# Optimization experiments

Hardware: AMD Instinct MI355X
Metric: run time of the kernel (lower is better)

Reference implementation:

```python
import jax, jax.numpy as jnp
import numpy as np

T, S, B, D, H, DH, DI = 1024, 1024, 4, 1024, 16, 64, 4096
SCALE = 1.0 / (DH ** 0.5)


def _ln(x, g, b, eps=1e-5):
    m = jnp.mean(x, axis=-1, keepdims=True)
    v = jnp.mean((x - m) ** 2, axis=-1, keepdims=True)
    return (x - m) * jax.lax.rsqrt(v + eps) * g + b


def setup_inputs() -> dict:
    key = jax.random.key(0)
    ks = jax.random.split(key, 16)
    s = 0.02
    inp = {
        "dec_inp": jax.random.normal(ks[0], (T, B, D), jnp.float32),
        "enc_out": jax.random.normal(ks[1], (T, B, D), jnp.float32),
        # causal mask for self-attn: [qlen, klen, bsz], True = masked
        "dec_mask": jnp.broadcast_to(jnp.triu(jnp.ones((T, T), bool), 1)[:, :, None], (T, T, B)),
        # encoder padding mask: [klen, bsz], last 128 positions padded
        "enc_mask": jnp.broadcast_to((jnp.arange(S) >= S - 128)[:, None], (S, B)),
        # self-attn params
        "W_q1": jax.random.normal(ks[2], (D, H * DH), jnp.float32) * s,
        "W_kv1": jax.random.normal(ks[3], (D, 2 * H * DH), jnp.float32) * s,
        "W_o1": jax.random.normal(ks[4], (H * DH, D), jnp.float32) * s,
        "g1": jnp.ones((D,), jnp.float32), "b1": jnp.zeros((D,), jnp.float32),
        # cross-attn params
        "W_q2": jax.random.normal(ks[5], (D, H * DH), jnp.float32) * s,
        "W_kv2": jax.random.normal(ks[6], (D, 2 * H * DH), jnp.float32) * s,
        "W_o2": jax.random.normal(ks[7], (H * DH, D), jnp.float32) * s,
        "g2": jnp.ones((D,), jnp.float32), "b2": jnp.zeros((D,), jnp.float32),
        # FFN params
        "W_ff1": jax.random.normal(ks[8], (D, DI), jnp.float32) * s,
        "b_ff1": jnp.zeros((DI,), jnp.float32),
        "W_ff2": jax.random.normal(ks[9], (DI, D), jnp.float32) * s,
        "b_ff2": jnp.zeros((D,), jnp.float32),
        "g3": jnp.ones((D,), jnp.float32), "b3": jnp.zeros((D,), jnp.float32),
    }
    return inp


def reference(dec_inp, enc_out, dec_mask, enc_mask,
              W_q1, W_kv1, W_o1, g1, b1,
              W_q2, W_kv2, W_o2, g2, b2,
              W_ff1, b_ff1, W_ff2, b_ff2, g3, b3):
    # ---- self-attention (MultiHeadAttn, pre_lnorm=True, mems=None) ----
    # NOTE: q is computed from the UN-normalized h; k,v from LN(c) — faithful to source.
    c = _ln(dec_inp, g1, b1)
    q = (dec_inp @ W_q1).reshape(T, B, H, DH)
    kv = (c @ W_kv1)
    k, v = jnp.split(kv, 2, axis=-1)
    k = k.reshape(T, B, H, DH)
    v = v.reshape(T, B, H, DH)
    score = jnp.einsum('ibnd,jbnd->ijbn', q, k) * SCALE  # [T,T,B,H]
    score = jnp.where(dec_mask[:, :, :, None], -jnp.inf, score)
    prob = jax.nn.softmax(score, axis=1)
    vec = jnp.einsum('ijbn,jbnd->ibnd', prob, v).reshape(T, B, H * DH)
    out1 = dec_inp + vec @ W_o1

    # ---- cross-attention (ContextMultiHeadAttn, pre_lnorm=True) ----
    # NOTE: residual uses the layer-normed h (source reassigns h = layer_norm(h)).
    h2 = _ln(out1, g2, b2)
    q2 = (h2 @ W_q2).reshape(T, B, H, DH)
    kv2 = enc_out @ W_kv2  # enc_out is NOT layer-normed in source
    k2, v2 = jnp.split(kv2, 2, axis=-1)
    k2 = k2.reshape(S, B, H, DH)
    v2 = v2.reshape(S, B, H, DH)
    score2 = jnp.einsum('ibnd,jbnd->ijbn', q2, k2) * SCALE  # [T,S,B,H]
    score2 = jnp.where(enc_mask[None, :, :, None], -10000.0, score2)
    prob2 = jax.nn.softmax(score2, axis=1)
    vec2 = jnp.einsum('ijbn,jbnd->ibnd', prob2, v2).reshape(T, B, H * DH)
    out2 = h2 + vec2 @ W_o2

    # ---- position-wise FFN (pre_lnorm) ----
    h3 = _ln(out2, g3, b3)
    core = jax.nn.gelu(h3 @ W_ff1 + b_ff1, approximate=False) @ W_ff2 + b_ff2
    return out2 + core
```

## Files before the change

### kernel.cpp

```cpp
#include <hip/hip_runtime.h>
#include <hip/hip_bf16.h>

#define T_ 1024
#define S_ 1024
#define B_ 4
#define D_ 1024
#define H_ 16
#define DH_ 64
#define DI_ 4096
#define NTOK 4096

typedef __attribute__((ext_vector_type(8))) short bf16x8;
typedef __attribute__((ext_vector_type(4))) float f32x4;

__device__ __forceinline__ short f2bf(float f) {
  unsigned u = __builtin_bit_cast(unsigned, f);
  u += 0x7fffu + ((u >> 16) & 1u);
  return (short)(u >> 16);
}

__device__ __forceinline__ void g2l16(const void* g, void* l) {
  __builtin_amdgcn_global_load_lds(
      (const __attribute__((address_space(1))) unsigned int*)g,
      (__attribute__((address_space(3))) unsigned int*)l, 16, 0, 0);
}

template <int EPI>
__global__ __launch_bounds__(256, 2) void gemm_bt(
    const short* __restrict__ A, const short* __restrict__ Bt,
    float* __restrict__ outF, short* __restrict__ outB,
    const float* __restrict__ res, const float* __restrict__ bias,
    short* __restrict__ Kgp, short* __restrict__ Vgp,
    int M, int N, int K) {
  __shared__ short sA[2][128 * 64];
  __shared__ short sB[2][128 * 64];
  const int tid = threadIdx.x;
  const int lane = tid & 63;
  const int w = tid >> 6;
  const int wr = w >> 1, wc = w & 1;
  const int r15 = lane & 15, g4 = lane >> 4;
  const size_t row0 = (size_t)blockIdx.x * 128;
  const size_t col0 = (size_t)blockIdx.y * 128;

  f32x4 acc[4][4];
#pragma unroll
  for (int i = 0; i < 4; i++)
#pragma unroll
    for (int j = 0; j < 4; j++) acc[i][j] = (f32x4){0.f, 0.f, 0.f, 0.f};

  auto stage = [&](int buf, int k0) {
#pragma unroll
    for (int i = 0; i < 4; i++) {
      int flat = i * 256 + tid;
      int row = flat >> 3;
      int gs = flat & 7;
      int col = k0 + ((gs ^ (row & 7)) << 3);
      g2l16(A + (row0 + row) * (size_t)K + col, &sA[buf][(i * 256 + w * 64) * 8]);
      g2l16(Bt + (col0 + row) * (size_t)K + col, &sB[buf][(i * 256 + w * 64) * 8]);
    }
  };

  stage(0, 0);
  __syncthreads();

  const int nk = K >> 6;
  for (int kt = 0; kt < nk; ++kt) {
    const int cur = kt & 1;
    if (kt + 1 < nk) stage(cur ^ 1, (kt + 1) << 6);
#pragma unroll
    for (int kk = 0; kk < 2; ++kk) {
      bf16x8 af[4], bfr[4];
#pragma unroll
      for (int mi = 0; mi < 4; mi++) {
        int rowA = wr * 64 + mi * 16 + r15;
        af[mi] = *(const bf16x8*)(&sA[cur][rowA * 64 +
                                           (((kk * 4 + g4) ^ (rowA & 7)) << 3)]);
        int rowB = wc * 64 + mi * 16 + r15;
        bfr[mi] = *(const bf16x8*)(&sB[cur][rowB * 64 +
                                            (((kk * 4 + g4) ^ (rowB & 7)) << 3)]);
      }
#pragma unroll
      for (int mi = 0; mi < 4; mi++)
#pragma unroll
        for (int ni = 0; ni < 4; ni++)
          acc[mi][ni] = __builtin_amdgcn_mfma_f32_16x16x32_bf16(af[mi], bfr[ni],
                                                                acc[mi][ni], 0, 0, 0);
    }
    __syncthreads();
  }

#pragma unroll
  for (int mi = 0; mi < 4; mi++) {
    size_t row = row0 + wr * 64 + mi * 16 + (g4 << 2);
#pragma unroll
    for (int ni = 0; ni < 4; ni++) {
      size_t col = col0 + wc * 64 + ni * 16 + r15;
      float bcol = (EPI == 2 || EPI == 3) ? bias[col] : 0.f;
#pragma unroll
      for (int r = 0; r < 4; r++) {
        size_t idx = (row + r) * (size_t)N + col;
        float v = acc[mi][ni][r];
        if (EPI == 0) {
          outB[idx] = f2bf(v);
        } else if (EPI == 1) {
          outF[idx] = v + res[idx];
        } else if (EPI == 2) {
          float x = v + bcol;
          float gl = 0.5f * x * (1.f + erff(x * 0.70710678118654752f));
          outB[idx] = f2bf(gl);
        } else if (EPI == 3) {
          outF[idx] = v + bcol + res[idx];
        } else {
          int tt = (int)(row + r) >> 2;
          int bb = (int)(row + r) & 3;
          int cc = (int)col;
          if (cc < 1024) {
            int hh = cc >> 6, dd = cc & 63;
            size_t base = (size_t)(bb * 16 + hh) * 65536 + (size_t)tt * 64;
            Kgp[base + ((((dd >> 3) ^ (tt & 7)) << 3) | (dd & 7))] = f2bf(v * 0.125f);
          } else {
            int hh = (cc >> 6) - 16, dd = cc & 63;
            size_t base = (size_t)(bb * 16 + hh) * 65536 + (size_t)(tt >> 6) * 4096;
            Vgp[base + ((tt >> 3) & 7) * 512 + dd * 8 + (tt & 7)] = f2bf(v);
          }
        }
      }
    }
  }
}

template <int MODE>
__global__ __launch_bounds__(256, 2) void attn_k2(const short* __restrict__ Qm,
                                                  const short* __restrict__ Kg,
                                                  const short* __restrict__ Vg,
                                                  short* __restrict__ Om) {
  __shared__ short Kl[2][4096];
  __shared__ short Vl[2][4096];
  __shared__ short Pl[4][2048];
  const int tid = threadIdx.x;
  const int lane = tid & 63;
  const int w = tid >> 6;
  const int r15 = lane & 15, g4 = lane >> 4;
  const int bh = blockIdx.x;
  const int qt = blockIdx.y;
  const int b = bh >> 4, h = bh & 15;
  const int qbase = qt * 128 + w * 32;
  const int ktDiag = qbase >> 6;

  bf16x8 qf[2][2];
#pragma unroll
  for (int g = 0; g < 2; g++)
#pragma unroll
    for (int hf = 0; hf < 2; hf++) {
      int row = qbase + g * 16 + r15;
      qf[g][hf] = *(const bf16x8*)(Qm + ((size_t)(row * 4 + b)) * 1024 + h * 64 +
                                   hf * 32 + g4 * 8);
    }

  const size_t kvbase = (size_t)bh * 65536;
  const int nkt = (MODE == 0) ? (2 * qt + 2) : 14;

  f32x4 o[2][4];
#pragma unroll
  for (int g = 0; g < 2; g++)
#pragma unroll
    for (int ni = 0; ni < 4; ni++) o[g][ni] = (f32x4){0.f, 0.f, 0.f, 0.f};
  float mrun[2][4], lrun[2][4];
#pragma unroll
  for (int g = 0; g < 2; g++)
#pragma unroll
    for (int r = 0; r < 4; r++) { mrun[g][r] = -1e30f; lrun[g][r] = 0.f; }

  {
    const size_t tb = kvbase;
#pragma unroll
    for (int i = 0; i < 2; i++) {
      g2l16(Kg + tb + (size_t)(i * 256 + tid) * 8, &Kl[0][(i * 256 + w * 64) * 8]);
      g2l16(Vg + tb + (size_t)(i * 256 + tid) * 8, &Vl[0][(i * 256 + w * 64) * 8]);
    }
  }
  __syncthreads();

  for (int kt = 0; kt < nkt; kt++) {
    const int cur = kt & 1;
    if (kt + 1 < nkt) {
      const size_t tb = kvbase + (size_t)(kt + 1) * 4096;
#pragma unroll
      for (int i = 0; i < 2; i++) {
        g2l16(Kg + tb + (size_t)(i * 256 + tid) * 8,
              &Kl[cur ^ 1][(i * 256 + w * 64) * 8]);
        g2l16(Vg + tb + (size_t)(i * 256 + tid) * 8,
              &Vl[cur ^ 1][(i * 256 + w * 64) * 8]);
      }
    }

    const bool active = (MODE == 1) || (kt * 64 <= qbase + 31);
    if (active) {
      bf16x8 kb[4][2];
#pragma unroll
      for (int ni = 0; ni < 4; ni++) {
        int row = ni * 16 + r15;
        kb[ni][0] = *(const bf16x8*)(&Kl[cur][row * 64 + ((g4 ^ (row & 7)) << 3)]);
        kb[ni][1] =
            *(const bf16x8*)(&Kl[cur][row * 64 + (((g4 + 4) ^ (row & 7)) << 3)]);
      }
      f32x4 sf[2][4];
#pragma unroll
      for (int g = 0; g < 2; g++)
#pragma unroll
        for (int ni = 0; ni < 4; ni++) {
          f32x4 s = (f32x4){0.f, 0.f, 0.f, 0.f};
          s = __builtin_amdgcn_mfma_f32_16x16x32_bf16(qf[g][0], kb[ni][0], s, 0, 0, 0);
          s = __builtin_amdgcn_mfma_f32_16x16x32_bf16(qf[g][1], kb[ni][1], s, 0, 0, 0);
          sf[g][ni] = s;
        }
      if (MODE == 0 && kt >= ktDiag) {
#pragma unroll
        for (int g = 0; g < 2; g++)
#pragma unroll
          for (int ni = 0; ni < 4; ni++)
#pragma unroll
            for (int r = 0; r < 4; r++) {
              int q = qbase + g * 16 + g4 * 4 + r;
              int key = kt * 64 + ni * 16 + r15;
              if (key > q) sf[g][ni][r] = -1e30f;
            }
      }
#pragma unroll
      for (int g = 0; g < 2; g++) {
        float corr[4];
#pragma unroll
        for (int r = 0; r < 4; r++) {
          float m = fmaxf(fmaxf(sf[g][0][r], sf[g][1][r]),
                          fmaxf(sf[g][2][r], sf[g][3][r]));
          m = fmaxf(m, __shfl_xor(m, 1));
          m = fmaxf(m, __shfl_xor(m, 2));
          m = fmaxf(m, __shfl_xor(m, 4));
          m = fmaxf(m, __shfl_xor(m, 8));
          float mn = fmaxf(mrun[g][r], m);
          corr[r] = __expf(mrun[g][r] - mn);
          mrun[g][r] = mn;
        }
        float rs[4] = {0.f, 0.f, 0.f, 0.f};
#pragma unroll
        for (int ni = 0; ni < 4; ni++)
#pragma unroll
          for (int r = 0; r < 4; r++) {
            float p = __expf(sf[g][ni][r] - mrun[g][r]);
            sf[g][ni][r] = p;
            rs[r] += p;
          }
#pragma unroll
        for (int r = 0; r < 4; r++) {
          rs[r] += __shfl_xor(rs[r], 1);
          rs[r] += __shfl_xor(rs[r], 2);
          rs[r] += __shfl_xor(rs[r], 4);
          rs[r] += __shfl_xor(rs[r], 8);
          lrun[g][r] = lrun[g][r] * corr[r] + rs[r];
        }
#pragma unroll
        for (int ni = 0; ni < 4; ni++)
#pragma unroll
          for (int r = 0; r < 4; r++) o[g][ni][r] *= corr[r];
#pragma unroll
        for (int ni = 0; ni < 4; ni++)
#pragma unroll
          for (int r = 0; r < 4; r++) {
            int qr = g * 16 + g4 * 4 + r;
            int key = ni * 16 + r15;
            Pl[w][qr * 64 + ((((key >> 3) ^ ((qr >> 1) & 7)) << 3) | (key & 7))] =
                f2bf(sf[g][ni][r]);
          }
      }
#pragma unroll
      for (int kk = 0; kk < 2; kk++) {
        int gw = kk * 4 + g4;
        bf16x8 pa0 = *(const bf16x8*)(&Pl[w][r15 * 64 + ((gw ^ ((r15 >> 1) & 7)) << 3)]);
        bf16x8 pa1 =
            *(const bf16x8*)(&Pl[w][(16 + r15) * 64 + ((gw ^ ((r15 >> 1) & 7)) << 3)]);
#pragma unroll
        for (int ni = 0; ni < 4; ni++) {
          bf16x8 vb = *(const bf16x8*)(&Vl[cur][(gw * 64 + ni * 16 + r15) * 8]);
          o[0][ni] = __builtin_amdgcn_mfma_f32_16x16x32_bf16(pa0, vb, o[0][ni], 0, 0, 0);
          o[1][ni] = __builtin_amdgcn_mfma_f32_16x16x32_bf16(pa1, vb, o[1][ni], 0, 0, 0);
        }
      }
    }
    __syncthreads();
  }

#pragma unroll
  for (int g = 0; g < 2; g++) {
    float inv[4];
#pragma unroll
    for (int r = 0; r < 4; r++) inv[r] = 1.f / lrun[g][r];
#pragma unroll
    for (int ni = 0; ni < 4; ni++) {
      int col = h * 64 + ni * 16 + r15;
#pragma unroll
      for (int r = 0; r < 4; r++) {
        int tg = qbase + g * 16 + g4 * 4 + r;
        Om[((size_t)(tg * 4 + b)) * 1024 + col] = f2bf(o[g][ni][r] * inv[r]);
      }
    }
  }
}

__global__ __launch_bounds__(256) void ln_k(const float* __restrict__ x,
                                            const float* __restrict__ gw,
                                            const float* __restrict__ bw,
                                            float* __restrict__ outF,
                                            short* __restrict__ outB,
                                            short* __restrict__ outXB) {
  const int row = blockIdx.x, tid = threadIdx.x;
  const float4 v = ((const float4*)(x + (size_t)row * 1024))[tid];
  float s = v.x + v.y + v.z + v.w;
  float ss = v.x * v.x + v.y * v.y + v.z * v.z + v.w * v.w;
#pragma unroll
  for (int d = 32; d >= 1; d >>= 1) {
    s += __shfl_xor(s, d);
    ss += __shfl_xor(ss, d);
  }
  __shared__ float red[8];
  const int w = tid >> 6;
  if ((tid & 63) == 0) { red[w] = s; red[4 + w] = ss; }
  __syncthreads();
  s = red[0] + red[1] + red[2] + red[3];
  ss = red[4] + red[5] + red[6] + red[7];
  const float mean = s * (1.f / 1024.f);
  const float var = ss * (1.f / 1024.f) - mean * mean;
  const float rstd = rsqrtf(var + 1e-5f);
  const float4 gv = ((const float4*)gw)[tid];
  const float4 bv = ((const float4*)bw)[tid];
  float4 y;
  y.x = (v.x - mean) * rstd * gv.x + bv.x;
  y.y = (v.y - mean) * rstd * gv.y + bv.y;
  y.z = (v.z - mean) * rstd * gv.z + bv.z;
  y.w = (v.w - mean) * rstd * gv.w + bv.w;
  if (outF) ((float4*)(outF + (size_t)row * 1024))[tid] = y;
  if (outB) {
    short4 ob;
    ob.x = f2bf(y.x); ob.y = f2bf(y.y); ob.z = f2bf(y.z); ob.w = f2bf(y.w);
    ((short4*)(outB + (size_t)row * 1024))[tid] = ob;
  }
  if (outXB) {
    short4 ob;
    ob.x = f2bf(v.x); ob.y = f2bf(v.y); ob.z = f2bf(v.z); ob.w = f2bf(v.w);
    ((short4*)(outXB + (size_t)row * 1024))[tid] = ob;
  }
}

__global__ __launch_bounds__(256) void cvt_bf16(const float* __restrict__ in,
                                                short* __restrict__ out) {
  const size_t i = (size_t)blockIdx.x * 256 + threadIdx.x;
  const float4 v = ((const float4*)in)[i];
  short4 ob;
  ob.x = f2bf(v.x); ob.y = f2bf(v.y); ob.z = f2bf(v.z); ob.w = f2bf(v.w);
  ((short4*)out)[i] = ob;
}

__global__ __launch_bounds__(256) void tr_cvt(const float* __restrict__ in,
                                              short* __restrict__ out, int K, int N) {
  __shared__ float t[64][65];
  const int tid = threadIdx.x;
  const int k0 = blockIdx.x * 64, n0 = blockIdx.y * 64;
#pragma unroll
  for (int i = 0; i < 16; i++) {
    int flat = i * 256 + tid;
    int r = flat >> 6, c = flat & 63;
    t[r][c] = in[(size_t)(k0 + r) * N + n0 + c];
  }
  __syncthreads();
#pragma unroll
  for (int i = 0; i < 16; i++) {
    int flat = i * 256 + tid;
    int r = flat >> 6, c = flat & 63;
    out[(size_t)(n0 + r) * K + k0 + c] = f2bf(t[c][r]);
  }
}

extern "C" void kernel_launch(void* const* d_in, const int* in_sizes, int n_in,
                              void* d_out, int out_size, void* d_ws, size_t ws_size,
                              hipStream_t stream) {
  const float* dec_inp = (const float*)d_in[0];
  const float* enc_out = (const float*)d_in[1];
  const float* W_q1 = (const float*)d_in[4];
  const float* W_kv1 = (const float*)d_in[5];
  const float* W_o1 = (const float*)d_in[6];
  const float* g1 = (const float*)d_in[7];
  const float* b1 = (const float*)d_in[8];
  const float* W_q2 = (const float*)d_in[9];
  const float* W_kv2 = (const float*)d_in[10];
  const float* W_o2 = (const float*)d_in[11];
  const float* g2 = (const float*)d_in[12];
  const float* b2 = (const float*)d_in[13];
  const float* W_ff1 = (const float*)d_in[14];
  const float* b_ff1 = (const float*)d_in[15];
  const float* W_ff2 = (const float*)d_in[16];
  const float* b_ff2 = (const float*)d_in[17];
  const float* g3 = (const float*)d_in[18];
  const float* b3 = (const float*)d_in[19];
  float* out = (float*)d_out;

  char* ws = (char*)d_ws;
  size_t off = 0;
  auto alloc = [&](size_t bytes) -> void* {
    void* p = ws + off;
    off += (bytes + 255) & ~(size_t)255;
    return p;
  };
  short* Wq1t = (short*)alloc(1024ull * 1024 * 2);
  short* Wkv1t = (short*)alloc(2048ull * 1024 * 2);
  short* Wo1t = (short*)alloc(1024ull * 1024 * 2);
  short* Wq2t = (short*)alloc(1024ull * 1024 * 2);
  short* Wkv2t = (short*)alloc(2048ull * 1024 * 2);
  short* Wo2t = (short*)alloc(1024ull * 1024 * 2);
  short* Wff1t = (short*)alloc(4096ull * 1024 * 2);
  short* Wff2t = (short*)alloc(1024ull * 4096 * 2);
  short* Xbf = (short*)alloc((size_t)NTOK * 1024 * 2);
  short* Ebf = (short*)alloc((size_t)NTOK * 1024 * 2);
  short* Cbf = (short*)alloc((size_t)NTOK * 1024 * 2);
  short* Qb = (short*)alloc((size_t)NTOK * 1024 * 2);
  short* Kg = (short*)alloc(64ull * 65536 * 2);
  short* Vg = (short*)alloc(64ull * 65536 * 2);
  short* VECb = (short*)alloc((size_t)NTOK * 1024 * 2);
  float* OUT1 = (float*)alloc((size_t)NTOK * 1024 * 4);
  float* H2f = (float*)alloc((size_t)NTOK * 1024 * 4);
  float* OUT2 = (float*)alloc((size_t)NTOK * 1024 * 4);
  short* FF1 = (short*)alloc((size_t)NTOK * 4096 * 2);
  short* H2b = Xbf;
  short* H3b = Cbf;

  dim3 blk(256, 1, 1);

  tr_cvt<<<dim3(16, 16), blk, 0, stream>>>(W_q1, Wq1t, 1024, 1024);
  tr_cvt<<<dim3(16, 32), blk, 0, stream>>>(W_kv1, Wkv1t, 1024, 2048);
  tr_cvt<<<dim3(16, 16), blk, 0, stream>>>(W_o1, Wo1t, 1024, 1024);
  tr_cvt<<<dim3(16, 16), blk, 0, stream>>>(W_q2, Wq2t, 1024, 1024);
  tr_cvt<<<dim3(16, 32), blk, 0, stream>>>(W_kv2, Wkv2t, 1024, 2048);
  tr_cvt<<<dim3(16, 16), blk, 0, stream>>>(W_o2, Wo2t, 1024, 1024);
  tr_cvt<<<dim3(16, 64), blk, 0, stream>>>(W_ff1, Wff1t, 1024, 4096);
  tr_cvt<<<dim3(64, 16), blk, 0, stream>>>(W_ff2, Wff2t, 4096, 1024);

  cvt_bf16<<<4096, blk, 0, stream>>>(enc_out, Ebf);
  ln_k<<<4096, blk, 0, stream>>>(dec_inp, g1, b1, nullptr, Cbf, Xbf);

  gemm_bt<0><<<dim3(32, 8), blk, 0, stream>>>(Xbf, Wq1t, nullptr, Qb, nullptr,
                                              nullptr, nullptr, nullptr, 4096, 1024, 1024);
  gemm_bt<4><<<dim3(32, 16), blk, 0, stream>>>(Cbf, Wkv1t, nullptr, nullptr, nullptr,
                                               nullptr, Kg, Vg, 4096, 2048, 1024);
  attn_k2<0><<<dim3(64, 8), blk, 0, stream>>>(Qb, Kg, Vg, VECb);
  gemm_bt<1><<<dim3(32, 8), blk, 0, stream>>>(VECb, Wo1t, OUT1, nullptr, dec_inp,
                                              nullptr, nullptr, nullptr, 4096, 1024, 1024);
  ln_k<<<4096, blk, 0, stream>>>(OUT1, g2, b2, H2f, H2b, nullptr);
  gemm_bt<0><<<dim3(32, 8), blk, 0, stream>>>(H2b, Wq2t, nullptr, Qb, nullptr,
                                              nullptr, nullptr, nullptr, 4096, 1024, 1024);
  gemm_bt<4><<<dim3(32, 16), blk, 0, stream>>>(Ebf, Wkv2t, nullptr, nullptr, nullptr,
                                               nullptr, Kg, Vg, 4096, 2048, 1024);
  attn_k2<1><<<dim3(64, 8), blk, 0, stream>>>(Qb, Kg, Vg, VECb);
  gemm_bt<1><<<dim3(32, 8), blk, 0, stream>>>(VECb, Wo2t, OUT2, nullptr, H2f,
                                              nullptr, nullptr, nullptr, 4096, 1024, 1024);
  ln_k<<<4096, blk, 0, stream>>>(OUT2, g3, b3, nullptr, H3b, nullptr);
  gemm_bt<2><<<dim3(32, 32), blk, 0, stream>>>(H3b, Wff1t, nullptr, FF1, nullptr,
                                               b_ff1, nullptr, nullptr, 4096, 4096, 1024);
  gemm_bt<3><<<dim3(32, 8), blk, 0, stream>>>(FF1, Wff2t, out, nullptr, OUT2,
                                              b_ff2, nullptr, nullptr, 4096, 1024, 4096);
}
```

Measured before the change: 378.4 us.

## Prefetch two tiles ahead with explicit vmcnt waits in GEMM and attention

Restructures the double-buffered LDS pipelines in the GEMM and attention kernels so two tiles are in flight. The next-next tile is issued right after the post-compute barrier, and s_waitcnt vmcnt with a count waits only for the older tile's loads. This replaces __syncthreads, which drains all outstanding global-to-LDS loads every iteration. The point is to overlap load latency with a full compute iteration. The cost is two barriers per iteration and correctness that depends on the hand-counted vmcnt values matching the number of issued loads.

```diff
diff --git a/kernel.cpp b/kernel.cpp
--- a/kernel.cpp
+++ b/kernel.cpp
@@ -48,25 +48,30 @@
 #pragma unroll
     for (int j = 0; j < 4; j++) acc[i][j] = (f32x4){0.f, 0.f, 0.f, 0.f};
 
-  auto stage = [&](int buf, int k0) {
+  auto stage = [&](int buf, int kt) {
+    const int k0 = kt << 6;
 #pragma unroll
     for (int i = 0; i < 4; i++) {
       int flat = i * 256 + tid;
       int row = flat >> 3;
-      int gs = flat & 7;
-      int col = k0 + ((gs ^ (row & 7)) << 3);
+      int col = k0 + (((flat & 7) ^ (row & 7)) << 3);
       g2l16(A + (row0 + row) * (size_t)K + col, &sA[buf][(i * 256 + w * 64) * 8]);
       g2l16(Bt + (col0 + row) * (size_t)K + col, &sB[buf][(i * 256 + w * 64) * 8]);
     }
   };
 
+  const int nk = K >> 6;
   stage(0, 0);
-  __syncthreads();
-
-  const int nk = K >> 6;
+  if (nk > 1) {
+    stage(1, 1);
+    asm volatile("s_waitcnt vmcnt(8)" ::: "memory");
+  } else {
+    asm volatile("s_waitcnt vmcnt(0)" ::: "memory");
+  }
+  __builtin_amdgcn_s_barrier();
+
   for (int kt = 0; kt < nk; ++kt) {
     const int cur = kt & 1;
-    if (kt + 1 < nk) stage(cur ^ 1, (kt + 1) << 6);
 #pragma unroll
     for (int kk = 0; kk < 2; ++kk) {
       bf16x8 af[4], bfr[4];
@@ -86,7 +91,16 @@
           acc[mi][ni] = __builtin_amdgcn_mfma_f32_16x16x32_bf16(af[mi], bfr[ni],
                                                                 acc[mi][ni], 0, 0, 0);
     }
-    __syncthreads();
+    asm volatile("" ::: "memory");
+    __builtin_amdgcn_s_barrier();
+    if (kt + 2 < nk) stage(cur, kt + 2);
+    if (kt + 1 < nk) {
+      if (kt + 2 < nk)
+        asm volatile("s_waitcnt vmcnt(8)" ::: "memory");
+      else
+        asm volatile("s_waitcnt vmcnt(0)" ::: "memory");
+      __builtin_amdgcn_s_barrier();
+    }
   }
 
 #pragma unroll
@@ -171,29 +185,26 @@
 #pragma unroll
     for (int r = 0; r < 4; r++) { mrun[g][r] = -1e30f; lrun[g][r] = 0.f; }
 
-  {
-    const size_t tb = kvbase;
+  auto stageKV = [&](int buf, int kt) {
+    const size_t tb = kvbase + (size_t)kt * 4096;
 #pragma unroll
     for (int i = 0; i < 2; i++) {
-      g2l16(Kg + tb + (size_t)(i * 256 + tid) * 8, &Kl[0][(i * 256 + w * 64) * 8]);
-      g2l16(Vg + tb + (size_t)(i * 256 + tid) * 8, &Vl[0][(i * 256 + w * 64) * 8]);
-    }
-  }
-  __syncthreads();
+      g2l16(Kg + tb + (size_t)(i * 256 + tid) * 8, &Kl[buf][(i * 256 + w * 64) * 8]);
+      g2l16(Vg + tb + (size_t)(i * 256 + tid) * 8, &Vl[buf][(i * 256 + w * 64) * 8]);
+    }
+  };
+
+  stageKV(0, 0);
+  if (nkt > 1) {
+    stageKV(1, 1);
+    asm volatile("s_waitcnt vmcnt(4)" ::: "memory");
+  } else {
+    asm volatile("s_waitcnt vmcnt(0)" ::: "memory");
+  }
+  __builtin_amdgcn_s_barrier();
 
   for (int kt = 0; kt < nkt; kt++) {
     const int cur = kt & 1;
-    if (kt + 1 < nkt) {
-      const size_t tb = kvbase + (size_t)(kt + 1) * 4096;
-#pragma unroll
-      for (int i = 0; i < 2; i++) {
-        g2l16(Kg + tb + (size_t)(i * 256 + tid) * 8,
-              &Kl[cur ^ 1][(i * 256 + w * 64) * 8]);
-        g2l16(Vg + tb + (size_t)(i * 256 + tid) * 8,
-              &Vl[cur ^ 1][(i * 256 + w * 64) * 8]);
-      }
-    }
-
     const bool active = (MODE == 1) || (kt * 64 <= qbase + 31);
     if (active) {
       bf16x8 kb[4][2];
@@ -286,7 +297,16 @@
         }
       }
     }
-    __syncthreads();
+    asm volatile("" ::: "memory");
+    __builtin_amdgcn_s_barrier();
+    if (kt + 2 < nkt) stageKV(cur, kt + 2);
+    if (kt + 1 < nkt) {
+      if (kt + 2 < nkt)
+        asm volatile("s_waitcnt vmcnt(4)" ::: "memory");
+      else
+        asm volatile("s_waitcnt vmcnt(0)" ::: "memory");
+      __builtin_amdgcn_s_barrier();
+    }
   }
 
 #pragma unroll
```

After: 388.7 us. 2.7% more time.
